# Kernel optimization log

Measured on AMD Instinct MI355X. Metric: run time of the kernel, lower is better.

Reference implementation:

```python
import jax, jax.numpy as jnp
import numpy as np

T = 5          # temporal frames
WS = 8         # window size (square)
HEADS = 6
DIM = 192      # output channels; qkv input channels = 3*DIM
SHIFT = WS // 2
HDIM = DIM // HEADS
SCALE = HDIM ** -0.5
N = T * WS * WS  # tokens per window = 320


def _rel_index():
    # Faithful replication of the torch buffer construction (including the
    # quirk that the dw channel gets no offset).
    coords = np.stack(np.meshgrid(np.arange(T), np.arange(WS), np.arange(WS), indexing='ij'))
    cf = coords.reshape(3, -1)                      # (3, N)
    rel = (cf[:, :, None] - cf[:, None, :]).transpose(1, 2, 0).astype(np.int64)
    rel[:, :, 0] += WS - 1                          # dt channel
    rel[:, :, 1] += WS - 1                          # dh channel
    rel[:, :, 0] *= 2 * WS - 1
    return rel.sum(-1)                               # (N, N) int

REL_INDEX = jnp.asarray(_rel_index())


def setup_inputs() -> dict:
    key = jax.random.key(0)
    k1, k2, k3, k4 = jax.random.split(key, 4)
    B, H, W = 2, 64, 64
    C = 3 * DIM
    qkv = jax.random.normal(k1, (B, T * H * W, C), jnp.float32)
    bias_table = jax.random.normal(k2, ((T * 2 * WS - 1) * (2 * WS - 1), HEADS), jnp.float32) * 0.02
    proj_w = jax.random.normal(k3, (DIM, DIM), jnp.float32) / np.sqrt(DIM)
    proj_b = jax.random.normal(k4, (DIM,), jnp.float32) * 0.01
    # Standard Swin shifted-window attention mask, tiled over T (t-outer order).
    img = np.zeros((H, W), np.float32)
    cnt = 0
    sls = (slice(0, -WS), slice(-WS, -SHIFT), slice(-SHIFT, None))
    for hs in sls:
        for ws_ in sls:
            img[hs, ws_] = cnt
            cnt += 1
    mw = img.reshape(H // WS, WS, W // WS, WS).transpose(0, 2, 1, 3).reshape(-1, WS * WS)
    mw = np.tile(mw, (1, T))                         # (nW, N)
    am = mw[:, None, :] - mw[:, :, None]
    mask = jnp.asarray(np.where(am != 0, -100.0, 0.0).astype(np.float32))
    return {'qkv': qkv, 'bias_table': bias_table, 'proj_w': proj_w,
            'proj_b': proj_b, 'mask': mask, 'H': H, 'W': W}


def reference(qkv, bias_table, proj_w, proj_b, mask, H, W):
    B, L, C = qkv.shape
    x = qkv.reshape(B, T, H, W, C)
    # cyclic shift
    x = jnp.roll(x, shift=(-SHIFT, -SHIFT), axis=(2, 3))
    # window partition -> (B*nW, N, C)
    x = x.reshape(B, T, H // WS, WS, W // WS, WS, C)
    x = x.transpose(0, 2, 4, 1, 3, 5, 6).reshape(-1, N, C)
    B_ = x.shape[0]
    qkv_ = x.reshape(B_, N, 3, HEADS, HDIM).transpose(2, 0, 3, 1, 4)  # (3,B_,h,N,d)
    q, k, v = qkv_[0] * SCALE, qkv_[1], qkv_[2]
    attn = jnp.einsum('bhqd,bhkd->bhqk', q, k)       # (B_, h, N, N)
    rpb = bias_table[REL_INDEX.reshape(-1)].reshape(N, N, HEADS).transpose(2, 0, 1)
    attn = attn + rpb[None]
    nW = mask.shape[0]
    attn = attn.reshape(B_ // nW, nW, HEADS, N, N) + mask[None, :, None]
    attn = jax.nn.softmax(attn.reshape(B_, HEADS, N, N), axis=-1)
    out = jnp.einsum('bhqk,bhkd->bhqd', attn, v)     # (B_, h, N, d)
    out = out.transpose(0, 2, 1, 3).reshape(B_, N, DIM)
    out = out @ proj_w.T + proj_b
    # window reverse -> (B, T, H, W, DIM)
    out = out.reshape(B, H // WS, W // WS, T, WS, WS, DIM)
    out = out.transpose(0, 3, 1, 4, 2, 5, 6).reshape(B, T, H, W, DIM)
    out = jnp.roll(out, shift=(SHIFT, SHIFT), axis=(2, 3))
    return out.reshape(B, T * H * W, DIM)
```

## Files before the change

### kernel.cpp

```cpp
#include <hip/hip_runtime.h>
#include <hip/hip_bf16.h>

#define TT      5
#define NHEADS  6
#define DIMC    192
#define SHIFT_  4
#define HDIM_   32
#define NTOK    320
#define NWIN    64
#define BATCH   2
#define LOG2E   1.44269504088896f
#define SCALE_LOG2E (0.17677669529663687f * 1.44269504088896f)
#define NEGMASK (-100.0f * 1.44269504088896f)

typedef short short8v __attribute__((ext_vector_type(8)));
typedef float floatx4 __attribute__((ext_vector_type(4)));
union FragU { uint4 u; short8v s; };

static __device__ __forceinline__ float bf16lo(unsigned u) {
    union { unsigned i; float f; } x; x.i = u << 16; return x.f;
}
static __device__ __forceinline__ float bf16hi(unsigned u) {
    union { unsigned i; float f; } x; x.i = u & 0xffff0000u; return x.f;
}
static __device__ __forceinline__ unsigned short bf16b(float f) {
    __hip_bfloat16 h = __float2bfloat16(f);
    unsigned short u; __builtin_memcpy(&u, &h, 2); return u;
}
static __device__ __forceinline__ unsigned pk2(float a, float b) {
    return (unsigned)bf16b(a) | ((unsigned)bf16b(b) << 16);
}
static __device__ __forceinline__ unsigned pk2h(float a, float b) {
    unsigned ua = __float_as_uint(a), ub = __float_as_uint(b);
    return ((ua + 0x8000u) >> 16) | ((ub + 0x8000u) & 0xffff0000u);
}
static __device__ __forceinline__ float fexp2(float x) {
    float r;
    asm("v_exp_f32 %0, %1" : "=v"(r) : "v"(x));
    return r;
}

static __device__ __forceinline__ bool detect_bf16(const unsigned* q) {
    uint4 w = ((const uint4*)q)[threadIdx.x & 63];
    int cnt = 0;
    unsigned e;
    e = (w.x >> 7) & 0xffu; cnt += (e >= 100u && e <= 135u);
    e = (w.y >> 7) & 0xffu; cnt += (e >= 100u && e <= 135u);
    e = (w.z >> 7) & 0xffu; cnt += (e >= 100u && e <= 135u);
    e = (w.w >> 7) & 0xffu; cnt += (e >= 100u && e <= 135u);
    unsigned long long m = __ballot(cnt >= 2);
    return __popcll(m) >= 32;
}

__global__ __launch_bounds__(NTOK) void attn_mfma(
    const void* __restrict__ qkv_raw,
    const float* __restrict__ rpb,
    __hip_bfloat16* __restrict__ win_out)
{
    const bool isbf = detect_bf16((const unsigned*)qkv_raw);
    const int b_  = blockIdx.x;
    const int h   = blockIdx.y;
    const int bb  = b_ >> 6;
    const int wdx = b_ & 63;
    const int wi  = wdx >> 3, wj = wdx & 7;
    const int tid = threadIdx.x;
    const int w    = tid >> 6;
    const int lane = tid & 63;
    const int l15  = lane & 15;
    const int quad = lane >> 4;
    const int g    = lane >> 3;
    const int li   = lane & 7;

    __shared__ unsigned short sK[320 * 40];
    __shared__ unsigned short sVT[32 * 328];

    {
        const int btok = w * 64;
        if (!isbf) {
            const float* q32 = (const float*)qkv_raw;
            #pragma unroll
            for (int r = 0; r < 8; r++) {
                const int token = btok + r * 8 + g;
                const int t = token >> 6, s = token & 63;
                const int gh = (wi * 8 + (s >> 3) + SHIFT_) & 63;
                const int gw = (wj * 8 + (s & 7) + SHIFT_) & 63;
                const long grow = (long)bb * (TT * 64 * 64) + t * 4096 + gh * 64 + gw;
                const float4 kv = *(const float4*)(q32 + grow * (3 * DIMC) + DIMC + h * HDIM_ + li * 4);
                const int l32 = token & 31;
                const int slot = (token & ~31) + ((l32 & 4) << 2) + ((l32 >> 3) << 2) + (l32 & 3);
                *(uint2*)&sK[slot * 40 + li * 4] = make_uint2(pk2(kv.x, kv.y), pk2(kv.z, kv.w));
            }
            #pragma unroll
            for (int r = 0; r < 8; r++) {
                const int token = btok + r * 8 + g;
                const int t = token >> 6, s = token & 63;
                const int gh = (wi * 8 + (s >> 3) + SHIFT_) & 63;
                const int gw = (wj * 8 + (s & 7) + SHIFT_) & 63;
                const long grow = (long)bb * (TT * 64 * 64) + t * 4096 + gh * 64 + gw;
                const float4 vv = *(const float4*)(q32 + grow * (3 * DIMC) + 2 * DIMC + h * HDIM_ + li * 4);
                const int d0 = li * 4;
                sVT[(d0 + 0) * 328 + token] = bf16b(vv.x);
                sVT[(d0 + 1) * 328 + token] = bf16b(vv.y);
                sVT[(d0 + 2) * 328 + token] = bf16b(vv.z);
                sVT[(d0 + 3) * 328 + token] = bf16b(vv.w);
            }
        } else {
            const unsigned short* q16 = (const unsigned short*)qkv_raw;
            #pragma unroll
            for (int r = 0; r < 8; r++) {
                const int token = btok + r * 8 + g;
                const int t = token >> 6, s = token & 63;
                const int gh = (wi * 8 + (s >> 3) + SHIFT_) & 63;
                const int gw = (wj * 8 + (s & 7) + SHIFT_) & 63;
                const long grow = (long)bb * (TT * 64 * 64) + t * 4096 + gh * 64 + gw;
                const uint2 kv = *(const uint2*)(q16 + grow * (3 * DIMC) + DIMC + h * HDIM_ + li * 4);
                const int l32 = token & 31;
                const int slot = (token & ~31) + ((l32 & 4) << 2) + ((l32 >> 3) << 2) + (l32 & 3);
                *(uint2*)&sK[slot * 40 + li * 4] = kv;
            }
            #pragma unroll
            for (int r = 0; r < 8; r++) {
                const int token = btok + r * 8 + g;
                const int t = token >> 6, s = token & 63;
                const int gh = (wi * 8 + (s >> 3) + SHIFT_) & 63;
                const int gw = (wj * 8 + (s & 7) + SHIFT_) & 63;
                const long grow = (long)bb * (TT * 64 * 64) + t * 4096 + gh * 64 + gw;
                const uint2 vv = *(const uint2*)(q16 + grow * (3 * DIMC) + 2 * DIMC + h * HDIM_ + li * 4);
                const int d0 = li * 4;
                sVT[(d0 + 0) * 328 + token] = (unsigned short)(vv.x & 0xffffu);
                sVT[(d0 + 1) * 328 + token] = (unsigned short)(vv.x >> 16);
                sVT[(d0 + 2) * 328 + token] = (unsigned short)(vv.y & 0xffffu);
                sVT[(d0 + 3) * 328 + token] = (unsigned short)(vv.y >> 16);
            }
        }
    }

    FragU qf[4];
    int labq[4];
    const float* rq[4];
    #pragma unroll
    for (int jq = 0; jq < 4; jq++) {
        const int qtok = w * 64 + jq * 16 + l15;
        const int t = qtok >> 6, s = qtok & 63, hl = s >> 3, wl = s & 7;
        rq[jq] = rpb + ((h * NTOK + qtok) * NTOK);
        const int hh = wi * 8 + hl, ww = wj * 8 + wl;
        labq[jq] = ((hh < 56) ? 0 : ((hh < 60) ? 1 : 2)) * 3 +
                   ((ww < 56) ? 0 : ((ww < 60) ? 1 : 2));
        const int gh = (wi * 8 + hl + SHIFT_) & 63;
        const int gw = (wj * 8 + wl + SHIFT_) & 63;
        const long grow = (long)bb * (TT * 64 * 64) + t * 4096 + gh * 64 + gw;
        if (!isbf) {
            const float* qp = (const float*)qkv_raw + grow * (3 * DIMC) + h * HDIM_ + quad * 8;
            qf[jq].u = make_uint4(
                pk2(qp[0]*SCALE_LOG2E, qp[1]*SCALE_LOG2E), pk2(qp[2]*SCALE_LOG2E, qp[3]*SCALE_LOG2E),
                pk2(qp[4]*SCALE_LOG2E, qp[5]*SCALE_LOG2E), pk2(qp[6]*SCALE_LOG2E, qp[7]*SCALE_LOG2E));
        } else {
            const uint4 uu = *(const uint4*)((const __hip_bfloat16*)qkv_raw + grow * (3 * DIMC) + h * HDIM_ + quad * 8);
            qf[jq].u = make_uint4(
                pk2(bf16lo(uu.x)*SCALE_LOG2E, bf16hi(uu.x)*SCALE_LOG2E),
                pk2(bf16lo(uu.y)*SCALE_LOG2E, bf16hi(uu.y)*SCALE_LOG2E),
                pk2(bf16lo(uu.z)*SCALE_LOG2E, bf16hi(uu.z)*SCALE_LOG2E),
                pk2(bf16lo(uu.w)*SCALE_LOG2E, bf16hi(uu.w)*SCALE_LOG2E));
        }
    }
    __syncthreads();

    const floatx4 z4 = {0.f, 0.f, 0.f, 0.f};
    floatx4 oacc[4][2];
    #pragma unroll
    for (int i = 0; i < 4; i++) { oacc[i][0] = z4; oacc[i][1] = z4; }
    float rs[4] = {0.f, 0.f, 0.f, 0.f};

    for (int kb = 0; kb < 10; kb++) {
        FragU kf0, kf1, vf0, vf1;
        kf0.u = *(const uint4*)&sK[(kb * 32 + l15) * 40 + quad * 8];
        kf1.u = *(const uint4*)&sK[(kb * 32 + 16 + l15) * 40 + quad * 8];
        vf0.u = *(const uint4*)&sVT[l15 * 328 + kb * 32 + quad * 8];
        vf1.u = *(const uint4*)&sVT[(16 + l15) * 328 + kb * 32 + quad * 8];

        float4 rb0[4], rb1[4];
        #pragma unroll
        for (int jq = 0; jq < 4; jq++) {
            const float* rp = rq[jq] + kb * 32 + quad * 8;
            rb0[jq] = *(const float4*)rp;
            rb1[jq] = *(const float4*)(rp + 4);
        }

        floatx4 sv0[4], sv1[4];
        #pragma unroll
        for (int jq = 0; jq < 4; jq++)
            sv0[jq] = __builtin_amdgcn_mfma_f32_16x16x32_bf16(kf0.s, qf[jq].s, z4, 0, 0, 0);
        #pragma unroll
        for (int jq = 0; jq < 4; jq++)
            sv1[jq] = __builtin_amdgcn_mfma_f32_16x16x32_bf16(kf1.s, qf[jq].s, z4, 0, 0, 0);

        const int sh   = (kb & 1) * 4 + quad;
        const int rhk  = (wi == 7) ? ((sh < 4) ? 1 : 2) : 0;
        const int lab0 = rhk * 3 + ((wj == 7) ? 1 : 0);
        const int lab1 = rhk * 3 + ((wj == 7) ? 2 : 0);

        #pragma unroll
        for (int jq = 0; jq < 4; jq++) {
            const float m0 = (lab0 != labq[jq]) ? NEGMASK : 0.f;
            const float m1 = (lab1 != labq[jq]) ? NEGMASK : 0.f;
            float e0[4], e1[4];
            e0[0] = fexp2(sv0[jq][0] + rb0[jq].x + m0);
            e0[1] = fexp2(sv0[jq][1] + rb0[jq].y + m0);
            e0[2] = fexp2(sv0[jq][2] + rb0[jq].z + m0);
            e0[3] = fexp2(sv0[jq][3] + rb0[jq].w + m0);
            e1[0] = fexp2(sv1[jq][0] + rb1[jq].x + m1);
            e1[1] = fexp2(sv1[jq][1] + rb1[jq].y + m1);
            e1[2] = fexp2(sv1[jq][2] + rb1[jq].z + m1);
            e1[3] = fexp2(sv1[jq][3] + rb1[jq].w + m1);
            rs[jq] += ((e0[0] + e0[1]) + (e0[2] + e0[3]))
                    + ((e1[0] + e1[1]) + (e1[2] + e1[3]));
            FragU pf;
            pf.u.x = pk2h(e0[0], e0[1]); pf.u.y = pk2h(e0[2], e0[3]);
            pf.u.z = pk2h(e1[0], e1[1]); pf.u.w = pk2h(e1[2], e1[3]);
            oacc[jq][0] = __builtin_amdgcn_mfma_f32_16x16x32_bf16(vf0.s, pf.s, oacc[jq][0], 0, 0, 0);
            oacc[jq][1] = __builtin_amdgcn_mfma_f32_16x16x32_bf16(vf1.s, pf.s, oacc[jq][1], 0, 0, 0);
        }
    }

    unsigned short* wp = (unsigned short*)win_out;
    #pragma unroll
    for (int jq = 0; jq < 4; jq++) {
        float r = rs[jq];
        r += __shfl_xor(r, 16);
        r += __shfl_xor(r, 32);
        const float inv = 1.0f / r;
        const long ob = ((long)b_ * NTOK + (w * 64 + jq * 16 + l15)) * DIMC + h * HDIM_ + quad * 4;
        #pragma unroll
        for (int nt = 0; nt < 2; nt++) {
            const floatx4 o = oacc[jq][nt];
            *(uint2*)&wp[ob + nt * 16] =
                make_uint2(pk2(o[0] * inv, o[1] * inv), pk2(o[2] * inv, o[3] * inv));
        }
    }
}

__global__ __launch_bounds__(256) void prep_all(
    const void* __restrict__ w_raw, const void* __restrict__ b_raw,
    const void* __restrict__ bias_raw,
    const unsigned* __restrict__ sniff,
    unsigned short* __restrict__ wbf, float* __restrict__ bf32,
    float* __restrict__ rpb)
{
    const bool isbf = detect_bf16(sniff);
    const int gid = blockIdx.x * 256 + threadIdx.x;
    if (gid < 36864) {
        if (!isbf) wbf[gid] = bf16b(((const float*)w_raw)[gid]);
        else       wbf[gid] = ((const unsigned short*)w_raw)[gid];
    }
    if (gid < 192) {
        bf32[gid] = isbf
            ? __bfloat162float(((const __hip_bfloat16*)b_raw)[gid])
            : ((const float*)b_raw)[gid];
    }
    const int q = gid / NTOK;
    const int k = gid - q * NTOK;
    const int cnq = (q >> 6) * 15 + ((q >> 3) & 7) + (q & 7);
    const int cnk = (k >> 6) * 15 + ((k >> 3) & 7) + (k & 7);
    const int idx = (cnq - cnk + 112) * NHEADS;
    #pragma unroll
    for (int h = 0; h < NHEADS; h++) {
        const float v = isbf
            ? __bfloat162float(((const __hip_bfloat16*)bias_raw)[idx + h])
            : ((const float*)bias_raw)[idx + h];
        rpb[(h * NTOK + q) * NTOK + k] = v * LOG2E;
    }
}

__global__ __launch_bounds__(256) void proj_mfma(
    const __hip_bfloat16* __restrict__ win,
    const unsigned short* __restrict__ wbf,
    const float* __restrict__ bf32,
    const unsigned* __restrict__ sniff,
    void* __restrict__ out_raw)
{
    const bool isbf = detect_bf16(sniff);
    const int tid  = threadIdx.x;
    const int w    = tid >> 6;
    const int lane = tid & 63;
    const int l15  = lane & 15;
    const int quad = lane >> 4;
    const int tok0 = blockIdx.x * 64 + w * 16;

    const floatx4 z4 = {0.f, 0.f, 0.f, 0.f};
    floatx4 acc[12];
    #pragma unroll
    for (int nt = 0; nt < 12; nt++) acc[nt] = z4;

    #pragma unroll
    for (int ks = 0; ks < 6; ks++) {
        FragU xf;
        xf.u = *(const uint4*)((const unsigned short*)win + ((long)tok0 + l15) * DIMC + ks * 32 + quad * 8);
        #pragma unroll
        for (int nt = 0; nt < 12; nt++) {
            FragU wf;
            wf.u = *(const uint4*)(wbf + (nt * 16 + l15) * DIMC + ks * 32 + quad * 8);
            acc[nt] = __builtin_amdgcn_mfma_f32_16x16x32_bf16(wf.s, xf.s, acc[nt], 0, 0, 0);
        }
    }

    const int token = tok0 + l15;
    const int bw = token / NTOK;
    const int nn = token - bw * NTOK;
    const int bb = bw >> 6, wdx = bw & 63, wi2 = wdx >> 3, wj2 = wdx & 7;
    const int t = nn >> 6, s2 = nn & 63, hl = s2 >> 3, wl = s2 & 7;
    const int gh = (wi2 * 8 + hl + SHIFT_) & 63;
    const int gw = (wj2 * 8 + wl + SHIFT_) & 63;
    const long rowoff = ((long)bb * (TT * 64 * 64) + t * 4096 + gh * 64 + gw) * DIMC;

    #pragma unroll
    for (int nt = 0; nt < 12; nt++) {
        const float4 bv = *(const float4*)&bf32[nt * 16 + quad * 4];
        const float o0 = acc[nt][0] + bv.x, o1 = acc[nt][1] + bv.y;
        const float o2 = acc[nt][2] + bv.z, o3 = acc[nt][3] + bv.w;
        const long off = rowoff + nt * 16 + quad * 4;
        if (!isbf) {
            *(float4*)((float*)out_raw + off) = make_float4(o0, o1, o2, o3);
        } else {
            *(uint2*)((unsigned short*)out_raw + off) = make_uint2(pk2(o0, o1), pk2(o2, o3));
        }
    }
}

extern "C" void kernel_launch(void* const* d_in, const int* in_sizes, int n_in,
                              void* d_out, int out_size, void* d_ws, size_t ws_size,
                              hipStream_t stream)
{
    (void)in_sizes; (void)n_in; (void)out_size; (void)ws_size;
    const void* qkv        = d_in[0];
    const void* bias_table = d_in[1];
    const void* proj_w     = d_in[2];
    const void* proj_b     = d_in[3];

    __hip_bfloat16* win = (__hip_bfloat16*)d_ws;
    unsigned short* wbf = (unsigned short*)((char*)d_ws + 15728640);
    float*          bfb = (float*)((char*)d_ws + 15802368);
    float*          rpb = (float*)((char*)d_ws + 15803136);

    prep_all<<<dim3(400), 256, 0, stream>>>(proj_w, proj_b, bias_table,
                                            (const unsigned*)qkv, wbf, bfb, rpb);
    attn_mfma<<<dim3(BATCH * NWIN, NHEADS), NTOK, 0, stream>>>(qkv, rpb, win);
    proj_mfma<<<dim3(BATCH * NWIN * NTOK / 64), 256, 0, stream>>>(
        win, wbf, bfb, (const unsigned*)qkv, d_out);
}
```

Measured before the change: 250.5 us.

## Stage K/V in two halves to halve attention LDS and add launch-bound hints

```diff
diff --git a/kernel.cpp b/kernel.cpp
--- a/kernel.cpp
+++ b/kernel.cpp
@@ -52,7 +52,7 @@
     return __popcll(m) >= 32;
 }
 
-__global__ __launch_bounds__(NTOK) void attn_mfma(
+__global__ __launch_bounds__(NTOK, 3) void attn_mfma(
     const void* __restrict__ qkv_raw,
     const float* __restrict__ rpb,
     __hip_bfloat16* __restrict__ win_out)
@@ -71,69 +71,8 @@
     const int g    = lane >> 3;
     const int li   = lane & 7;
 
-    __shared__ unsigned short sK[320 * 40];
-    __shared__ unsigned short sVT[32 * 328];
-
-    {
-        const int btok = w * 64;
-        if (!isbf) {
-            const float* q32 = (const float*)qkv_raw;
-            #pragma unroll
-            for (int r = 0; r < 8; r++) {
-                const int token = btok + r * 8 + g;
-                const int t = token >> 6, s = token & 63;
-                const int gh = (wi * 8 + (s >> 3) + SHIFT_) & 63;
-                const int gw = (wj * 8 + (s & 7) + SHIFT_) & 63;
-                const long grow = (long)bb * (TT * 64 * 64) + t * 4096 + gh * 64 + gw;
-                const float4 kv = *(const float4*)(q32 + grow * (3 * DIMC) + DIMC + h * HDIM_ + li * 4);
-                const int l32 = token & 31;
-                const int slot = (token & ~31) + ((l32 & 4) << 2) + ((l32 >> 3) << 2) + (l32 & 3);
-                *(uint2*)&sK[slot * 40 + li * 4] = make_uint2(pk2(kv.x, kv.y), pk2(kv.z, kv.w));
-            }
-            #pragma unroll
-            for (int r = 0; r < 8; r++) {
-                const int token = btok + r * 8 + g;
-                const int t = token >> 6, s = token & 63;
-                const int gh = (wi * 8 + (s >> 3) + SHIFT_) & 63;
-                const int gw = (wj * 8 + (s & 7) + SHIFT_) & 63;
-                const long grow = (long)bb * (TT * 64 * 64) + t * 4096 + gh * 64 + gw;
-                const float4 vv = *(const float4*)(q32 + grow * (3 * DIMC) + 2 * DIMC + h * HDIM_ + li * 4);
-                const int d0 = li * 4;
-                sVT[(d0 + 0) * 328 + token] = bf16b(vv.x);
-                sVT[(d0 + 1) * 328 + token] = bf16b(vv.y);
-                sVT[(d0 + 2) * 328 + token] = bf16b(vv.z);
-                sVT[(d0 + 3) * 328 + token] = bf16b(vv.w);
-            }
-        } else {
-            const unsigned short* q16 = (const unsigned short*)qkv_raw;
-            #pragma unroll
-            for (int r = 0; r < 8; r++) {
-                const int token = btok + r * 8 + g;
-                const int t = token >> 6, s = token & 63;
-                const int gh = (wi * 8 + (s >> 3) + SHIFT_) & 63;
-                const int gw = (wj * 8 + (s & 7) + SHIFT_) & 63;
-                const long grow = (long)bb * (TT * 64 * 64) + t * 4096 + gh * 64 + gw;
-                const uint2 kv = *(const uint2*)(q16 + grow * (3 * DIMC) + DIMC + h * HDIM_ + li * 4);
-                const int l32 = token & 31;
-                const int slot = (token & ~31) + ((l32 & 4) << 2) + ((l32 >> 3) << 2) + (l32 & 3);
-                *(uint2*)&sK[slot * 40 + li * 4] = kv;
-            }
-            #pragma unroll
-            for (int r = 0; r < 8; r++) {
-                const int token = btok + r * 8 + g;
-                const int t = token >> 6, s = token & 63;
-                const int gh = (wi * 8 + (s >> 3) + SHIFT_) & 63;
-                const int gw = (wj * 8 + (s & 7) + SHIFT_) & 63;
-                const long grow = (long)bb * (TT * 64 * 64) + t * 4096 + gh * 64 + gw;
-                const uint2 vv = *(const uint2*)(q16 + grow * (3 * DIMC) + 2 * DIMC + h * HDIM_ + li * 4);
-                const int d0 = li * 4;
-                sVT[(d0 + 0) * 328 + token] = (unsigned short)(vv.x & 0xffffu);
-                sVT[(d0 + 1) * 328 + token] = (unsigned short)(vv.x >> 16);
-                sVT[(d0 + 2) * 328 + token] = (unsigned short)(vv.y & 0xffffu);
-                sVT[(d0 + 3) * 328 + token] = (unsigned short)(vv.y >> 16);
-            }
-        }
-    }
+    __shared__ unsigned short sK[160 * 40];
+    __shared__ unsigned short sVT[32 * 168];
 
     FragU qf[4];
     int labq[4];
@@ -163,7 +102,6 @@
                 pk2(bf16lo(uu.w)*SCALE_LOG2E, bf16hi(uu.w)*SCALE_LOG2E));
         }
     }
-    __syncthreads();
 
     const floatx4 z4 = {0.f, 0.f, 0.f, 0.f};
     floatx4 oacc[4][2];
@@ -171,54 +109,125 @@
     for (int i = 0; i < 4; i++) { oacc[i][0] = z4; oacc[i][1] = z4; }
     float rs[4] = {0.f, 0.f, 0.f, 0.f};
 
-    for (int kb = 0; kb < 10; kb++) {
-        FragU kf0, kf1, vf0, vf1;
-        kf0.u = *(const uint4*)&sK[(kb * 32 + l15) * 40 + quad * 8];
-        kf1.u = *(const uint4*)&sK[(kb * 32 + 16 + l15) * 40 + quad * 8];
-        vf0.u = *(const uint4*)&sVT[l15 * 328 + kb * 32 + quad * 8];
-        vf1.u = *(const uint4*)&sVT[(16 + l15) * 328 + kb * 32 + quad * 8];
-
-        float4 rb0[4], rb1[4];
-        #pragma unroll
-        for (int jq = 0; jq < 4; jq++) {
-            const float* rp = rq[jq] + kb * 32 + quad * 8;
-            rb0[jq] = *(const float4*)rp;
-            rb1[jq] = *(const float4*)(rp + 4);
-        }
-
-        floatx4 sv0[4], sv1[4];
-        #pragma unroll
-        for (int jq = 0; jq < 4; jq++)
-            sv0[jq] = __builtin_amdgcn_mfma_f32_16x16x32_bf16(kf0.s, qf[jq].s, z4, 0, 0, 0);
-        #pragma unroll
-        for (int jq = 0; jq < 4; jq++)
-            sv1[jq] = __builtin_amdgcn_mfma_f32_16x16x32_bf16(kf1.s, qf[jq].s, z4, 0, 0, 0);
-
-        const int sh   = (kb & 1) * 4 + quad;
-        const int rhk  = (wi == 7) ? ((sh < 4) ? 1 : 2) : 0;
-        const int lab0 = rhk * 3 + ((wj == 7) ? 1 : 0);
-        const int lab1 = rhk * 3 + ((wj == 7) ? 2 : 0);
-
-        #pragma unroll
-        for (int jq = 0; jq < 4; jq++) {
-            const float m0 = (lab0 != labq[jq]) ? NEGMASK : 0.f;
-            const float m1 = (lab1 != labq[jq]) ? NEGMASK : 0.f;
-            float e0[4], e1[4];
-            e0[0] = fexp2(sv0[jq][0] + rb0[jq].x + m0);
-            e0[1] = fexp2(sv0[jq][1] + rb0[jq].y + m0);
-            e0[2] = fexp2(sv0[jq][2] + rb0[jq].z + m0);
-            e0[3] = fexp2(sv0[jq][3] + rb0[jq].w + m0);
-            e1[0] = fexp2(sv1[jq][0] + rb1[jq].x + m1);
-            e1[1] = fexp2(sv1[jq][1] + rb1[jq].y + m1);
-            e1[2] = fexp2(sv1[jq][2] + rb1[jq].z + m1);
-            e1[3] = fexp2(sv1[jq][3] + rb1[jq].w + m1);
-            rs[jq] += ((e0[0] + e0[1]) + (e0[2] + e0[3]))
-                    + ((e1[0] + e1[1]) + (e1[2] + e1[3]));
-            FragU pf;
-            pf.u.x = pk2h(e0[0], e0[1]); pf.u.y = pk2h(e0[2], e0[3]);
-            pf.u.z = pk2h(e1[0], e1[1]); pf.u.w = pk2h(e1[2], e1[3]);
-            oacc[jq][0] = __builtin_amdgcn_mfma_f32_16x16x32_bf16(vf0.s, pf.s, oacc[jq][0], 0, 0, 0);
-            oacc[jq][1] = __builtin_amdgcn_mfma_f32_16x16x32_bf16(vf1.s, pf.s, oacc[jq][1], 0, 0, 0);
+    for (int half = 0; half < 2; half++) {
+        if (half) __syncthreads();
+
+        {
+            const int btok = w * 32;
+            if (!isbf) {
+                const float* q32 = (const float*)qkv_raw;
+                #pragma unroll
+                for (int r = 0; r < 4; r++) {
+                    const int ltok = btok + r * 8 + g;
+                    const int token = half * 160 + ltok;
+                    const int t = token >> 6, s = token & 63;
+                    const int gh = (wi * 8 + (s >> 3) + SHIFT_) & 63;
+                    const int gw = (wj * 8 + (s & 7) + SHIFT_) & 63;
+                    const long grow = (long)bb * (TT * 64 * 64) + t * 4096 + gh * 64 + gw;
+                    const float4 kv = *(const float4*)(q32 + grow * (3 * DIMC) + DIMC + h * HDIM_ + li * 4);
+                    const int l32 = ltok & 31;
+                    const int slot = (ltok & ~31) + ((l32 & 4) << 2) + ((l32 >> 3) << 2) + (l32 & 3);
+                    *(uint2*)&sK[slot * 40 + li * 4] = make_uint2(pk2(kv.x, kv.y), pk2(kv.z, kv.w));
+                }
+                #pragma unroll
+                for (int r = 0; r < 4; r++) {
+                    const int ltok = btok + r * 8 + g;
+                    const int token = half * 160 + ltok;
+                    const int t = token >> 6, s = token & 63;
+                    const int gh = (wi * 8 + (s >> 3) + SHIFT_) & 63;
+                    const int gw = (wj * 8 + (s & 7) + SHIFT_) & 63;
+                    const long grow = (long)bb * (TT * 64 * 64) + t * 4096 + gh * 64 + gw;
+                    const float4 vv = *(const float4*)(q32 + grow * (3 * DIMC) + 2 * DIMC + h * HDIM_ + li * 4);
+                    const int d0 = li * 4;
+                    sVT[(d0 + 0) * 168 + ltok] = bf16b(vv.x);
+                    sVT[(d0 + 1) * 168 + ltok] = bf16b(vv.y);
+                    sVT[(d0 + 2) * 168 + ltok] = bf16b(vv.z);
+                    sVT[(d0 + 3) * 168 + ltok] = bf16b(vv.w);
+                }
+            } else {
+                const unsigned short* q16 = (const unsigned short*)qkv_raw;
+                #pragma unroll
+                for (int r = 0; r < 4; r++) {
+                    const int ltok = btok + r * 8 + g;
+                    const int token = half * 160 + ltok;
+                    const int t = token >> 6, s = token & 63;
+                    const int gh = (wi * 8 + (s >> 3) + SHIFT_) & 63;
+                    const int gw = (wj * 8 + (s & 7) + SHIFT_) & 63;
+                    const long grow = (long)bb * (TT * 64 * 64) + t * 4096 + gh * 64 + gw;
+                    const uint2 kv = *(const uint2*)(q16 + grow * (3 * DIMC) + DIMC + h * HDIM_ + li * 4);
+                    const int l32 = ltok & 31;
+                    const int slot = (ltok & ~31) + ((l32 & 4) << 2) + ((l32 >> 3) << 2) + (l32 & 3);
+                    *(uint2*)&sK[slot * 40 + li * 4] = kv;
+                }
+                #pragma unroll
+                for (int r = 0; r < 4; r++) {
+                    const int ltok = btok + r * 8 + g;
+                    const int token = half * 160 + ltok;
+                    const int t = token >> 6, s = token & 63;
+                    const int gh = (wi * 8 + (s >> 3) + SHIFT_) & 63;
+                    const int gw = (wj * 8 + (s & 7) + SHIFT_) & 63;
+                    const long grow = (long)bb * (TT * 64 * 64) + t * 4096 + gh * 64 + gw;
+                    const uint2 vv = *(const uint2*)(q16 + grow * (3 * DIMC) + 2 * DIMC + h * HDIM_ + li * 4);
+                    const int d0 = li * 4;
+                    sVT[(d0 + 0) * 168 + ltok] = (unsigned short)(vv.x & 0xffffu);
+                    sVT[(d0 + 1) * 168 + ltok] = (unsigned short)(vv.x >> 16);
+                    sVT[(d0 + 2) * 168 + ltok] = (unsigned short)(vv.y & 0xffffu);
+                    sVT[(d0 + 3) * 168 + ltok] = (unsigned short)(vv.y >> 16);
+                }
+            }
+        }
+        __syncthreads();
+
+        for (int kbl = 0; kbl < 5; kbl++) {
+            const int kb = half * 5 + kbl;
+            FragU kf0, kf1, vf0, vf1;
+            kf0.u = *(const uint4*)&sK[(kbl * 32 + l15) * 40 + quad * 8];
+            kf1.u = *(const uint4*)&sK[(kbl * 32 + 16 + l15) * 40 + quad * 8];
+            vf0.u = *(const uint4*)&sVT[l15 * 168 + kbl * 32 + quad * 8];
+            vf1.u = *(const uint4*)&sVT[(16 + l15) * 168 + kbl * 32 + quad * 8];
+
+            float4 rb0[4], rb1[4];
+            #pragma unroll
+            for (int jq = 0; jq < 4; jq++) {
+                const float* rp = rq[jq] + kb * 32 + quad * 8;
+                rb0[jq] = *(const float4*)rp;
+                rb1[jq] = *(const float4*)(rp + 4);
+            }
+
+            floatx4 sv0[4], sv1[4];
+            #pragma unroll
+            for (int jq = 0; jq < 4; jq++)
+                sv0[jq] = __builtin_amdgcn_mfma_f32_16x16x32_bf16(kf0.s, qf[jq].s, z4, 0, 0, 0);
+            #pragma unroll
+            for (int jq = 0; jq < 4; jq++)
+                sv1[jq] = __builtin_amdgcn_mfma_f32_16x16x32_bf16(kf1.s, qf[jq].s, z4, 0, 0, 0);
+
+            const int sh   = (kb & 1) * 4 + quad;
+            const int rhk  = (wi == 7) ? ((sh < 4) ? 1 : 2) : 0;
+            const int lab0 = rhk * 3 + ((wj == 7) ? 1 : 0);
+            const int lab1 = rhk * 3 + ((wj == 7) ? 2 : 0);
+
+            #pragma unroll
+            for (int jq = 0; jq < 4; jq++) {
+                const float m0 = (lab0 != labq[jq]) ? NEGMASK : 0.f;
+                const float m1 = (lab1 != labq[jq]) ? NEGMASK : 0.f;
+                float e0[4], e1[4];
+                e0[0] = fexp2(sv0[jq][0] + rb0[jq].x + m0);
+                e0[1] = fexp2(sv0[jq][1] + rb0[jq].y + m0);
+                e0[2] = fexp2(sv0[jq][2] + rb0[jq].z + m0);
+                e0[3] = fexp2(sv0[jq][3] + rb0[jq].w + m0);
+                e1[0] = fexp2(sv1[jq][0] + rb1[jq].x + m1);
+                e1[1] = fexp2(sv1[jq][1] + rb1[jq].y + m1);
+                e1[2] = fexp2(sv1[jq][2] + rb1[jq].z + m1);
+                e1[3] = fexp2(sv1[jq][3] + rb1[jq].w + m1);
+                rs[jq] += ((e0[0] + e0[1]) + (e0[2] + e0[3]))
+                        + ((e1[0] + e1[1]) + (e1[2] + e1[3]));
+                FragU pf;
+                pf.u.x = pk2h(e0[0], e0[1]); pf.u.y = pk2h(e0[2], e0[3]);
+                pf.u.z = pk2h(e1[0], e1[1]); pf.u.w = pk2h(e1[2], e1[3]);
+                oacc[jq][0] = __builtin_amdgcn_mfma_f32_16x16x32_bf16(vf0.s, pf.s, oacc[jq][0], 0, 0, 0);
+                oacc[jq][1] = __builtin_amdgcn_mfma_f32_16x16x32_bf16(vf1.s, pf.s, oacc[jq][1], 0, 0, 0);
+            }
         }
     }
 
@@ -271,7 +280,7 @@
     }
 }
 
-__global__ __launch_bounds__(256) void proj_mfma(
+__global__ __launch_bounds__(256, 4) void proj_mfma(
     const __hip_bfloat16* __restrict__ win,
     const unsigned short* __restrict__ wbf,
     const float* __restrict__ bf32,
```

Result: slower. 342.6 us (+36.7%).
